# Optimization experiments

Hardware: AMD Instinct MI355X
Metric: run time of the kernel (lower is better)

Reference implementation:

```python
import jax, jax.numpy as jnp
import numpy as np

DIM = 1024
N_HEADS = 16
B, S = 2, 2048


def setup_inputs() -> dict:
    key = jax.random.key(0)
    ks = jax.random.split(key, 9)
    scale = 1.0 / np.sqrt(DIM)
    return {
        "i1": jax.random.normal(ks[0], (B, S, DIM), jnp.float32),
        "i2": jax.random.normal(ks[1], (B, S, DIM), jnp.float32),
        "cr": jax.random.normal(ks[2], (B, S, 2), jnp.float32),
        # Linear params stored as [in, out] so forward is x @ W + b (same math as torch x W^T + b)
        "Wq": jax.random.normal(ks[3], (DIM, DIM), jnp.float32) * scale,
        "bq": jnp.zeros((DIM,), jnp.float32),
        "Wkv": jax.random.normal(ks[4], (DIM, 2 * DIM), jnp.float32) * scale,
        "bkv": jnp.zeros((2 * DIM,), jnp.float32),
        "Wmo": jax.random.normal(ks[5], (2, DIM), jnp.float32) * (1.0 / np.sqrt(2.0)),
        "bmo": jnp.zeros((DIM,), jnp.float32),
    }


def reference(i1, i2, cr, Wq, bq, Wkv, bkv, Wmo, bmo):
    H = N_HEADS
    Dh = DIM // H
    b, s, _ = i1.shape

    q = (i1 @ Wq + bq).reshape(b, s, H, Dh)                # [B,S,H,Dh]
    kv = i2 @ Wkv + bkv                                     # [B,S,2*DIM]
    k = kv[..., :DIM].reshape(b, s, H, Dh)
    v = kv[..., DIM:].reshape(b, s, H, Dh)
    mo = (cr @ Wmo + bmo).reshape(b, s, H, Dh)              # [B,S,H,Dh]

    scores = jnp.einsum("bqhd,bkhd->bhqk", q, k) / jnp.sqrt(jnp.asarray(Dh, q.dtype))
    probs = jax.nn.softmax(scores, axis=-1)                 # [B,H,S,S] (dropout p=0)

    h = jnp.einsum("bhqk,bkhd->bqhd", probs, v).reshape(b, s, DIM)
    m = jnp.einsum("bhqk,bkhd->bqhd", probs, mo).reshape(b, s, DIM)
    return h, m
```

## Files before the change

kernel.cpp:

```cpp
#include <hip/hip_runtime.h>
#include <hip/hip_bf16.h>

typedef __attribute__((ext_vector_type(8))) short short8;
typedef __attribute__((ext_vector_type(4))) short short4_t;
typedef __attribute__((ext_vector_type(4))) float f32x4;
typedef unsigned short ushort_t;

#define DEV __device__ __forceinline__

DEV ushort_t f2bf(float f) {
    unsigned u = __builtin_bit_cast(unsigned, f);
    u = u + 0x7fffu + ((u >> 16) & 1u);
    return (ushort_t)(u >> 16);
}

DEV unsigned pk_bf16(float lo, float hi) {
    __hip_bfloat162 h = __float22bfloat162_rn(make_float2(lo, hi));
    unsigned u;
    __builtin_memcpy(&u, &h, sizeof(u));
    return u;
}

DEV float fast_exp2(float x) {
#if __has_builtin(__builtin_amdgcn_exp2f)
    return __builtin_amdgcn_exp2f(x);
#else
    float r;
    asm("v_exp_f32 %0, %1" : "=v"(r) : "v"(x));
    return r;
#endif
}

DEV short8 ld8(const ushort_t* p) { return *reinterpret_cast<const short8*>(p); }

#define SCL_F 0.18033688011112042f

__global__ __launch_bounds__(256)
void cvt_bf16(const float* __restrict__ in, ushort_t* __restrict__ out)
{
    const size_t i = ((size_t)blockIdx.x * 256 + threadIdx.x) * 8;
    const float4 a = *reinterpret_cast<const float4*>(in + i);
    const float4 b = *reinterpret_cast<const float4*>(in + i + 4);
    short8 v;
    v[0] = (short)f2bf(a.x); v[1] = (short)f2bf(a.y);
    v[2] = (short)f2bf(a.z); v[3] = (short)f2bf(a.w);
    v[4] = (short)f2bf(b.x); v[5] = (short)f2bf(b.y);
    v[6] = (short)f2bf(b.z); v[7] = (short)f2bf(b.w);
    *reinterpret_cast<short8*>(out + i) = v;
}

__global__ __launch_bounds__(256)
void tcvt_bf16(const float* __restrict__ W, ushort_t* __restrict__ Wt, int K, int N)
{
    __shared__ ushort_t tile[64][72];
    const int t = threadIdx.x;
    const int nx = blockIdx.x * 64, ky = blockIdx.y * 64;
    const int r = t >> 2, q = (t & 3) * 16;

    const float* src = W + (size_t)(ky + r) * N + nx + q;
#pragma unroll
    for (int i = 0; i < 4; ++i) {
        const float4 v = *reinterpret_cast<const float4*>(src + 4 * i);
        tile[r][q + 4 * i + 0] = f2bf(v.x);
        tile[r][q + 4 * i + 1] = f2bf(v.y);
        tile[r][q + 4 * i + 2] = f2bf(v.z);
        tile[r][q + 4 * i + 3] = f2bf(v.w);
    }
    __syncthreads();
    short8 o0, o1;
#pragma unroll
    for (int i = 0; i < 8; ++i) {
        o0[i] = (short)tile[q + i][r];
        o1[i] = (short)tile[q + 8 + i][r];
    }
    ushort_t* dst = Wt + (size_t)(nx + r) * K + ky + q;
    *reinterpret_cast<short8*>(dst) = o0;
    *reinterpret_cast<short8*>(dst + 8) = o1;
}

__global__ __launch_bounds__(256, 2)
void proj_all(const ushort_t* __restrict__ A1, const ushort_t* __restrict__ A2,
              const ushort_t* __restrict__ Wqt, const ushort_t* __restrict__ Wkvt,
              const float* __restrict__ bqv, const float* __restrict__ bkv,
              ushort_t* __restrict__ Qr, ushort_t* __restrict__ Kr,
              ushort_t* __restrict__ Vt)
{
    __shared__ ushort_t As[128 * 72];
    __shared__ ushort_t Bs[128 * 72];

    const int t = threadIdx.x;
    const int lane = t & 63;
    const int wv = t >> 6;
    const int wr = wv >> 1, wc = wv & 1;
    const int c = lane & 15, g = lane >> 4;
    const int m0 = blockIdx.y * 128;
    const int nblk = blockIdx.x;

    const ushort_t* A;
    const ushort_t* Wt;
    const float* bias;
    int n0;
    if (nblk < 8) { A = A1; Wt = Wqt;  bias = bqv; n0 = nblk * 128; }
    else          { A = A2; Wt = Wkvt; bias = bkv; n0 = (nblk - 8) * 128; }
    const bool isQ = (nblk < 8);
    const float qscale = isQ ? SCL_F : 1.0f;

    f32x4 acc[4][4];
    const f32x4 zero4 = {0.f, 0.f, 0.f, 0.f};
#pragma unroll
    for (int mi = 0; mi < 4; ++mi)
#pragma unroll
        for (int ni = 0; ni < 4; ++ni) acc[mi][ni] = zero4;

    const int srow[4] = { (t + 0)   >> 3, (t + 256) >> 3, (t + 512) >> 3, (t + 768) >> 3 };
    const int skq     = (t & 7) * 8;

    short8 a_reg[4], b_reg[4];
#pragma unroll
    for (int rep = 0; rep < 4; ++rep) {
        a_reg[rep] = ld8(A  + (size_t)(m0 + srow[rep]) * 1024 + skq);
        b_reg[rep] = ld8(Wt + (size_t)(n0 + srow[rep]) * 1024 + skq);
    }

    for (int it = 0; it < 16; ++it) {
#pragma unroll
        for (int rep = 0; rep < 4; ++rep) {
            *reinterpret_cast<short8*>(&As[srow[rep] * 72 + skq]) = a_reg[rep];
            *reinterpret_cast<short8*>(&Bs[srow[rep] * 72 + skq]) = b_reg[rep];
        }
        __syncthreads();
        if (it < 15) {
            const int k1 = (it + 1) * 64;
#pragma unroll
            for (int rep = 0; rep < 4; ++rep) {
                a_reg[rep] = ld8(A  + (size_t)(m0 + srow[rep]) * 1024 + k1 + skq);
                b_reg[rep] = ld8(Wt + (size_t)(n0 + srow[rep]) * 1024 + k1 + skq);
            }
        }
#pragma unroll
        for (int kk = 0; kk < 64; kk += 32) {
            short8 afr[4], bfr[4];
#pragma unroll
            for (int mi = 0; mi < 4; ++mi)
                afr[mi] = ld8(&As[(wr * 64 + mi * 16 + c) * 72 + kk + 8 * g]);
#pragma unroll
            for (int ni = 0; ni < 4; ++ni)
                bfr[ni] = ld8(&Bs[(wc * 64 + ni * 16 + c) * 72 + kk + 8 * g]);
#pragma unroll
            for (int mi = 0; mi < 4; ++mi)
#pragma unroll
                for (int ni = 0; ni < 4; ++ni)
                    acc[mi][ni] = __builtin_amdgcn_mfma_f32_16x16x32_bf16(
                        afr[mi], bfr[ni], acc[mi][ni], 0, 0, 0);
        }
        __syncthreads();
    }

#pragma unroll
    for (int mi = 0; mi < 4; ++mi) {
#pragma unroll
        for (int ni = 0; ni < 4; ++ni) {
            const int n = n0 + wc * 64 + ni * 16 + c;
            const float bb = bias[n];
#pragma unroll
            for (int j = 0; j < 4; ++j) {
                const int m = m0 + wr * 64 + mi * 16 + 4 * g + j;
                const int b = m >> 11, s = m & 2047;
                const ushort_t val = f2bf((acc[mi][ni][j] + bb) * qscale);
                if (isQ) {
                    Qr[((size_t)((b * 16 + (n >> 6)) * 2048 + s)) * 64 + (n & 63)] = val;
                } else if (n < 1024) {
                    Kr[((size_t)((b * 16 + (n >> 6)) * 2048 + s)) * 64 + (n & 63)] = val;
                } else {
                    const int np = n - 1024;
                    Vt[(size_t)((b * 16 + (np >> 6)) * 64 + (np & 63)) * 2048 + s] = val;
                }
            }
        }
    }
}

__global__ __launch_bounds__(256)
void proj_gemm(const float* __restrict__ A, const float* __restrict__ W,
               const float* __restrict__ bias, int N,
               ushort_t* __restrict__ outRow, ushort_t* __restrict__ outT)
{
    __shared__ ushort_t As[128 * 72];
    __shared__ ushort_t Bt[128 * 72];

    const int t = threadIdx.x;
    const int lane = t & 63;
    const int wv = t >> 6;
    const int wr = wv >> 1, wc = wv & 1;
    const int c = lane & 15, g = lane >> 4;
    const int m0 = blockIdx.y * 128, n0 = blockIdx.x * 128;
    const float qscale = (outT == nullptr) ? SCL_F : 1.0f;

    f32x4 acc[4][4];
    const f32x4 zero4 = {0.f, 0.f, 0.f, 0.f};
#pragma unroll
    for (int mi = 0; mi < 4; ++mi)
#pragma unroll
        for (int ni = 0; ni < 4; ++ni) acc[mi][ni] = zero4;

    for (int it = 0; it < 16; ++it) {
        const int k0 = it * 64;
        {
            const int kq = (t & 15) * 4;
            int r = t >> 4;
#pragma unroll
            for (int rep = 0; rep < 8; ++rep, r += 16) {
                float4 v = *reinterpret_cast<const float4*>(
                    A + (size_t)(m0 + r) * 1024 + k0 + kq);
                ushort_t* dst = &As[r * 72 + kq];
                dst[0] = f2bf(v.x); dst[1] = f2bf(v.y);
                dst[2] = f2bf(v.z); dst[3] = f2bf(v.w);
            }
        }
        {
            const int nq = (t & 31) * 4;
            const int kr = t >> 5;
#pragma unroll
            for (int rep = 0; rep < 8; ++rep) {
                const int k = kr + 8 * rep;
                float4 v = *reinterpret_cast<const float4*>(
                    W + (size_t)(k0 + k) * N + n0 + nq);
                Bt[(nq + 0) * 72 + k] = f2bf(v.x);
                Bt[(nq + 1) * 72 + k] = f2bf(v.y);
                Bt[(nq + 2) * 72 + k] = f2bf(v.z);
                Bt[(nq + 3) * 72 + k] = f2bf(v.w);
            }
        }
        __syncthreads();
#pragma unroll
        for (int kk = 0; kk < 64; kk += 32) {
            short8 afr[4], bfr[4];
#pragma unroll
            for (int mi = 0; mi < 4; ++mi)
                afr[mi] = ld8(&As[(wr * 64 + mi * 16 + c) * 72 + kk + 8 * g]);
#pragma unroll
            for (int ni = 0; ni < 4; ++ni)
                bfr[ni] = ld8(&Bt[(wc * 64 + ni * 16 + c) * 72 + kk + 8 * g]);
#pragma unroll
            for (int mi = 0; mi < 4; ++mi)
#pragma unroll
                for (int ni = 0; ni < 4; ++ni)
                    acc[mi][ni] = __builtin_amdgcn_mfma_f32_16x16x32_bf16(
                        afr[mi], bfr[ni], acc[mi][ni], 0, 0, 0);
        }
        __syncthreads();
    }

#pragma unroll
    for (int mi = 0; mi < 4; ++mi) {
#pragma unroll
        for (int ni = 0; ni < 4; ++ni) {
            const int n = n0 + wc * 64 + ni * 16 + c;
            const float bb = bias[n];
#pragma unroll
            for (int j = 0; j < 4; ++j) {
                const int m = m0 + wr * 64 + mi * 16 + 4 * g + j;
                const int b = m >> 11, s = m & 2047;
                const ushort_t val = f2bf((acc[mi][ni][j] + bb) * qscale);
                if (outT != nullptr && n >= 1024) {
                    const int np = n - 1024;
                    const int hh = np >> 6, d = np & 63;
                    outT[(size_t)((b * 16 + hh) * 64 + d) * 2048 + s] = val;
                } else {
                    const int hh = n >> 6, d = n & 63;
                    outRow[((size_t)((b * 16 + hh) * 2048 + s)) * 64 + d] = val;
                }
            }
        }
    }
}

DEV void tile_compute(const ushort_t* __restrict__ Ks, const ushort_t* __restrict__ Vs,
                      const ushort_t* __restrict__ Sts, int c, int g,
                      const short8 (&bq)[2][2],
                      f32x4 (&accv)[2][4], f32x4 (&stat)[2])
{
    const f32x4 zero4 = {0.f, 0.f, 0.f, 0.f};
    const int kxor = (c & 7) << 3;
    const int vxor = (c & 7) << 2;

    short8 KC[2][2];
#pragma unroll
    for (int ct = 0; ct < 2; ++ct)
#pragma unroll
        for (int st = 0; st < 2; ++st)
            KC[ct][st] = ld8(&Ks[(ct * 16 + c) * 64 + ((st * 32 + 8 * g) ^ kxor)]);
    short8 VC[4];
#pragma unroll
    for (int dt = 0; dt < 4; ++dt) {
        const short4_t vlo = *reinterpret_cast<const short4_t*>(
            &Vs[(dt * 16 + c) * 32 + ((4 * g) ^ vxor)]);
        const short4_t vhi = *reinterpret_cast<const short4_t*>(
            &Vs[(dt * 16 + c) * 32 + ((4 * g + 16) ^ vxor)]);
        VC[dt] = __builtin_shufflevector(vlo, vhi, 0, 1, 2, 3, 4, 5, 6, 7);
    }
    const short4_t slo = *reinterpret_cast<const short4_t*>(
        &Sts[c * 32 + ((4 * g) ^ vxor)]);
    const short4_t shi = *reinterpret_cast<const short4_t*>(
        &Sts[c * 32 + ((4 * g + 16) ^ vxor)]);
    const short8 stf = __builtin_shufflevector(slo, shi, 0, 1, 2, 3, 4, 5, 6, 7);

    f32x4 sc[2][2];
#pragma unroll
    for (int qt = 0; qt < 2; ++qt)
#pragma unroll
        for (int ct = 0; ct < 2; ++ct) {
            f32x4 z = zero4;
            z = __builtin_amdgcn_mfma_f32_16x16x32_bf16(KC[ct][0], bq[qt][0], z, 0, 0, 0);
            z = __builtin_amdgcn_mfma_f32_16x16x32_bf16(KC[ct][1], bq[qt][1], z, 0, 0, 0);
            sc[qt][ct] = z;
        }

    short8 pa[2];
#pragma unroll
    for (int qt = 0; qt < 2; ++qt) {
        float e[2][4];
#pragma unroll
        for (int ct = 0; ct < 2; ++ct)
#pragma unroll
            for (int j = 0; j < 4; ++j)
                e[ct][j] = fast_exp2(sc[qt][ct][j]);
        int4 w;
        w.x = (int)pk_bf16(e[0][0], e[0][1]);
        w.y = (int)pk_bf16(e[0][2], e[0][3]);
        w.z = (int)pk_bf16(e[1][0], e[1][1]);
        w.w = (int)pk_bf16(e[1][2], e[1][3]);
        pa[qt] = __builtin_bit_cast(short8, w);
    }

#pragma unroll
    for (int qt = 0; qt < 2; ++qt)
        stat[qt] = __builtin_amdgcn_mfma_f32_16x16x32_bf16(stf, pa[qt], stat[qt], 0, 0, 0);
#pragma unroll
    for (int dt = 0; dt < 4; ++dt) {
        accv[0][dt] = __builtin_amdgcn_mfma_f32_16x16x32_bf16(VC[dt], pa[0], accv[0][dt], 0, 0, 0);
        accv[1][dt] = __builtin_amdgcn_mfma_f32_16x16x32_bf16(VC[dt], pa[1], accv[1][dt], 0, 0, 0);
    }
}

DEV void pair_body(const ushort_t* __restrict__ Kh, const ushort_t* __restrict__ Vh,
                   const float* __restrict__ crb, int kvA, int kvB,
                   const ushort_t* KsC0, const ushort_t* VsC0, const ushort_t* StC0,
                   const ushort_t* KsC1, const ushort_t* VsC1, const ushort_t* StC1,
                   ushort_t* KsN0, ushort_t* VsN0, ushort_t* StN0,
                   ushort_t* KsN1, ushort_t* VsN1, ushort_t* StN1,
                   int t, int c, int g, int rk, int ck, int rv, int cv,
                   int kaddr, int vaddr0, int vaddr1,
                   const short8 (&bq)[2][2],
                   f32x4 (&accv)[2][4], f32x4 (&stat)[2])
{
    const short8 kregA = ld8(Kh + (size_t)(kvA + rk) * 64 + ck);
    const short8 vregA = ld8(Vh + (size_t)rv * 2048 + kvA + cv);
    const short8 kregB = ld8(Kh + (size_t)(kvB + rk) * 64 + ck);
    const short8 vregB = ld8(Vh + (size_t)rv * 2048 + kvB + cv);
    ushort_t crsh = 0; int staddr = 0;
    if (t < 128) {
        const int kvX = (t & 64) ? kvB : kvA;
        const int row = 1 + ((t >> 5) & 1);
        const float v = crb[(size_t)(kvX + (t & 31)) * 2 + (row - 1)];
        crsh = f2bf(v);
        staddr = row * 32 + ((t & 31) ^ ((row & 7) << 2));
    }
    __builtin_amdgcn_sched_barrier(0);

    tile_compute(KsC0, VsC0, StC0, c, g, bq, accv, stat);
    tile_compute(KsC1, VsC1, StC1, c, g, bq, accv, stat);

    *reinterpret_cast<short8*>(&KsN0[kaddr]) = kregA;
    *reinterpret_cast<short8*>(&KsN1[kaddr]) = kregB;
    *reinterpret_cast<short4_t*>(&VsN0[vaddr0]) = __builtin_shufflevector(vregA, vregA, 0, 1, 2, 3);
    *reinterpret_cast<short4_t*>(&VsN0[vaddr1]) = __builtin_shufflevector(vregA, vregA, 4, 5, 6, 7);
    *reinterpret_cast<short4_t*>(&VsN1[vaddr0]) = __builtin_shufflevector(vregB, vregB, 0, 1, 2, 3);
    *reinterpret_cast<short4_t*>(&VsN1[vaddr1]) = __builtin_shufflevector(vregB, vregB, 4, 5, 6, 7);
    if (t < 128) ((t & 64) ? StN1 : StN0)[staddr] = crsh;
    __syncthreads();
}

__global__ __launch_bounds__(256, 2)
void attn_kernel(const ushort_t* __restrict__ Qr, const ushort_t* __restrict__ Kr,
                 const ushort_t* __restrict__ Vt, const float* __restrict__ cr,
                 const float* __restrict__ Wmo, const float* __restrict__ bmo,
                 float* __restrict__ out)
{
    __shared__ ushort_t smem[18432];
    ushort_t* K0 = smem;            ushort_t* K1 = smem + 2048;
    ushort_t* K2 = smem + 4096;     ushort_t* K3 = smem + 6144;
    ushort_t* V0 = smem + 8192;     ushort_t* V1 = smem + 10240;
    ushort_t* V2 = smem + 12288;    ushort_t* V3 = smem + 14336;
    ushort_t* S0 = smem + 16384;    ushort_t* S1 = smem + 16896;
    ushort_t* S2 = smem + 17408;    ushort_t* S3 = smem + 17920;

    const int t = threadIdx.x;
    const int w = t >> 6, lane = t & 63;
    const int c = lane & 15, g = lane >> 4;
    const int rk = t >> 3, ck = (t & 7) * 8;
    const int rv = t >> 2, cv = (t & 3) * 8;
    const int kaddr  = rk * 64 + (ck ^ ((rk & 7) << 3));
    const int vaddr0 = rv * 32 + (cv ^ ((rv & 7) << 2));
    const int vaddr1 = rv * 32 + ((cv + 4) ^ ((rv & 7) << 2));

    const int gid = blockIdx.x;
    const int bh = (gid & 7) + 8 * ((gid >> 3) & 3);
    const int xt = gid >> 5;
    const int b = bh >> 4, hh = bh & 15;
    const int qb = xt * 128 + w * 32;

    const ushort_t* Qh = Qr + (size_t)bh * (2048 * 64);
    const ushort_t* Kh = Kr + (size_t)bh * (2048 * 64);
    const ushort_t* Vh = Vt + (size_t)bh * (64 * 2048);
    const float*   crb = cr + (size_t)b * (2048 * 2);

    short8 bq[2][2];
#pragma unroll
    for (int qt = 0; qt < 2; ++qt)
#pragma unroll
        for (int st = 0; st < 2; ++st)
            bq[qt][st] = ld8(Qh + (size_t)(qb + qt * 16 + c) * 64 + st * 32 + 8 * g);

    f32x4 accv[2][4];
    f32x4 stat[2];
    const f32x4 zero4 = {0.f, 0.f, 0.f, 0.f};
#pragma unroll
    for (int qt = 0; qt < 2; ++qt) {
        stat[qt] = zero4;
#pragma unroll
        for (int dt = 0; dt < 4; ++dt) accv[qt][dt] = zero4;
    }

    for (int idx = t; idx < 2048; idx += 256) {
        const int row = (idx >> 5) & 15;
        if (row != 1 && row != 2)
            smem[16384 + idx] = (row == 0) ? (ushort_t)0x3F80 : (ushort_t)0;
    }

    {
        const short8 kA = ld8(Kh + (size_t)rk * 64 + ck);
        const short8 vA = ld8(Vh + (size_t)rv * 2048 + cv);
        const short8 kB = ld8(Kh + (size_t)(32 + rk) * 64 + ck);
        const short8 vB = ld8(Vh + (size_t)rv * 2048 + 32 + cv);
        *reinterpret_cast<short8*>(&K0[kaddr]) = kA;
        *reinterpret_cast<short8*>(&K1[kaddr]) = kB;
        *reinterpret_cast<short4_t*>(&V0[vaddr0]) = __builtin_shufflevector(vA, vA, 0, 1, 2, 3);
        *reinterpret_cast<short4_t*>(&V0[vaddr1]) = __builtin_shufflevector(vA, vA, 4, 5, 6, 7);
        *reinterpret_cast<short4_t*>(&V1[vaddr0]) = __builtin_shufflevector(vB, vB, 0, 1, 2, 3);
        *reinterpret_cast<short4_t*>(&V1[vaddr1]) = __builtin_shufflevector(vB, vB, 4, 5, 6, 7);
        if (t < 128) {
            const int kvX = (t & 64) ? 32 : 0;
            const int row = 1 + ((t >> 5) & 1);
            const float v = crb[(size_t)(kvX + (t & 31)) * 2 + (row - 1)];
            ((t & 64) ? S1 : S0)[row * 32 + ((t & 31) ^ ((row & 7) << 2))] = f2bf(v);
        }
    }
    __syncthreads();

    for (int i = 0; i < 16; ++i) {
        const int base = i * 128;
        pair_body(Kh, Vh, crb, base + 64, base + 96,
                  K0, V0, S0, K1, V1, S1,
                  K2, V2, S2, K3, V3, S3,
                  t, c, g, rk, ck, rv, cv, kaddr, vaddr0, vaddr1,
                  bq, accv, stat);
        pair_body(Kh, Vh, crb, (base + 128) & 2047, (base + 160) & 2047,
                  K2, V2, S2, K3, V3, S3,
                  K0, V0, S0, K1, V1, S1,
                  t, c, g, rk, ck, rv, cv, kaddr, vaddr0, vaddr1,
                  bq, accv, stat);
    }

    float lst[2], a0s[2], a1s[2];
#pragma unroll
    for (int qt = 0; qt < 2; ++qt) {
        lst[qt] = __shfl(stat[qt][0], c, 64);
        a0s[qt] = __shfl(stat[qt][1], c, 64);
        a1s[qt] = __shfl(stat[qt][2], c, 64);
    }

#pragma unroll
    for (int qt = 0; qt < 2; ++qt) {
        const int q = qb + qt * 16 + c;
        const float inv = 1.f / lst[qt];
        const float a0 = a0s[qt] * inv, a1 = a1s[qt] * inv;
#pragma unroll
        for (int dt = 0; dt < 4; ++dt) {
            const int d = hh * 64 + dt * 16 + 4 * g;
            const float4 w0 = *reinterpret_cast<const float4*>(Wmo + d);
            const float4 w1 = *reinterpret_cast<const float4*>(Wmo + 1024 + d);
            const float4 bm = *reinterpret_cast<const float4*>(bmo + d);
            const size_t oidx = ((size_t)(b * 2048 + q)) * 1024 + d;
            float4 hv, mv;
            hv.x = accv[qt][dt][0] * inv; hv.y = accv[qt][dt][1] * inv;
            hv.z = accv[qt][dt][2] * inv; hv.w = accv[qt][dt][3] * inv;
            mv.x = a0 * w0.x + a1 * w1.x + bm.x;
            mv.y = a0 * w0.y + a1 * w1.y + bm.y;
            mv.z = a0 * w0.z + a1 * w1.z + bm.z;
            mv.w = a0 * w0.w + a1 * w1.w + bm.w;
            *reinterpret_cast<float4*>(out + oidx) = hv;
            *reinterpret_cast<float4*>(out + 4194304 + oidx) = mv;
        }
    }
}

extern "C" void kernel_launch(void* const* d_in, const int* in_sizes, int n_in,
                              void* d_out, int out_size, void* d_ws, size_t ws_size,
                              hipStream_t stream)
{
    const float* i1  = (const float*)d_in[0];
    const float* i2  = (const float*)d_in[1];
    const float* cr  = (const float*)d_in[2];
    const float* Wq  = (const float*)d_in[3];
    const float* bq  = (const float*)d_in[4];
    const float* Wkv = (const float*)d_in[5];
    const float* bkv = (const float*)d_in[6];
    const float* Wmo = (const float*)d_in[7];
    const float* bmo = (const float*)d_in[8];
    float* out = (float*)d_out;

    ushort_t* Qr = (ushort_t*)d_ws;
    ushort_t* Kr = Qr + 4194304;
    ushort_t* Vt = Kr + 4194304;

    if (ws_size >= 48234496ULL) {
        ushort_t* A1   = Vt + 4194304;
        ushort_t* A2   = A1 + 4194304;
        ushort_t* Wqt  = A2 + 4194304;
        ushort_t* Wkvt = Wqt + 1048576;
        cvt_bf16<<<dim3(2048), dim3(256), 0, stream>>>(i1, A1);
        cvt_bf16<<<dim3(2048), dim3(256), 0, stream>>>(i2, A2);
        tcvt_bf16<<<dim3(16, 16), dim3(256), 0, stream>>>(Wq, Wqt, 1024, 1024);
        tcvt_bf16<<<dim3(32, 16), dim3(256), 0, stream>>>(Wkv, Wkvt, 1024, 2048);
        proj_all<<<dim3(24, 32), dim3(256), 0, stream>>>(A1, A2, Wqt, Wkvt, bq, bkv, Qr, Kr, Vt);
    } else {
        proj_gemm<<<dim3(8, 32), dim3(256), 0, stream>>>(i1, Wq, bq, 1024, Qr, nullptr);
        proj_gemm<<<dim3(16, 32), dim3(256), 0, stream>>>(i2, Wkv, bkv, 2048, Kr, Vt);
    }
    attn_kernel<<<dim3(512), dim3(256), 0, stream>>>(Qr, Kr, Vt, cr, Wmo, bmo, out);
}
```

Before: 115.7 us.

## Fuse fp32-to-bf16 activation conversion into projection GEMM and add MFMA priority hints

Drops the two standalone cvt_bf16 kernels. proj_all now loads fp32 activations directly and packs them to bf16 while staging them into shared memory, which removes a full write and re-read of two 16 MB-scale intermediates plus two launches. The cost is that proj_all reloads fp32 A tiles from global memory for each of its 24 column blocks, doubling the A-tile bytes per load and raising register pressure for the prefetch. The attention inner loop also wraps its MFMA sections in s_setprio to favour matrix issue over the exp and pack work.

Result: slower. 119.1 us (+2.9%).

```diff
diff --git a/kernel.cpp b/kernel.cpp
--- a/kernel.cpp
+++ b/kernel.cpp
@@ -36,20 +36,6 @@
 #define SCL_F 0.18033688011112042f
 
 __global__ __launch_bounds__(256)
-void cvt_bf16(const float* __restrict__ in, ushort_t* __restrict__ out)
-{
-    const size_t i = ((size_t)blockIdx.x * 256 + threadIdx.x) * 8;
-    const float4 a = *reinterpret_cast<const float4*>(in + i);
-    const float4 b = *reinterpret_cast<const float4*>(in + i + 4);
-    short8 v;
-    v[0] = (short)f2bf(a.x); v[1] = (short)f2bf(a.y);
-    v[2] = (short)f2bf(a.z); v[3] = (short)f2bf(a.w);
-    v[4] = (short)f2bf(b.x); v[5] = (short)f2bf(b.y);
-    v[6] = (short)f2bf(b.z); v[7] = (short)f2bf(b.w);
-    *reinterpret_cast<short8*>(out + i) = v;
-}
-
-__global__ __launch_bounds__(256)
 void tcvt_bf16(const float* __restrict__ W, ushort_t* __restrict__ Wt, int K, int N)
 {
     __shared__ ushort_t tile[64][72];
@@ -79,7 +65,7 @@
 }
 
 __global__ __launch_bounds__(256, 2)
-void proj_all(const ushort_t* __restrict__ A1, const ushort_t* __restrict__ A2,
+void proj_all(const float* __restrict__ i1, const float* __restrict__ i2,
               const ushort_t* __restrict__ Wqt, const ushort_t* __restrict__ Wkvt,
               const float* __restrict__ bqv, const float* __restrict__ bkv,
               ushort_t* __restrict__ Qr, ushort_t* __restrict__ Kr,
@@ -96,12 +82,12 @@
     const int m0 = blockIdx.y * 128;
     const int nblk = blockIdx.x;
 
-    const ushort_t* A;
+    const float* Af;
     const ushort_t* Wt;
     const float* bias;
     int n0;
-    if (nblk < 8) { A = A1; Wt = Wqt;  bias = bqv; n0 = nblk * 128; }
-    else          { A = A2; Wt = Wkvt; bias = bkv; n0 = (nblk - 8) * 128; }
+    if (nblk < 8) { Af = i1; Wt = Wqt;  bias = bqv; n0 = nblk * 128; }
+    else          { Af = i2; Wt = Wkvt; bias = bkv; n0 = (nblk - 8) * 128; }
     const bool isQ = (nblk < 8);
     const float qscale = isQ ? SCL_F : 1.0f;
 
@@ -115,17 +101,26 @@
     const int srow[4] = { (t + 0)   >> 3, (t + 256) >> 3, (t + 512) >> 3, (t + 768) >> 3 };
     const int skq     = (t & 7) * 8;
 
-    short8 a_reg[4], b_reg[4];
+    float4 a_lo[4], a_hi[4];
+    short8 b_reg[4];
 #pragma unroll
     for (int rep = 0; rep < 4; ++rep) {
-        a_reg[rep] = ld8(A  + (size_t)(m0 + srow[rep]) * 1024 + skq);
+        const float* src = Af + (size_t)(m0 + srow[rep]) * 1024 + skq;
+        a_lo[rep] = *reinterpret_cast<const float4*>(src);
+        a_hi[rep] = *reinterpret_cast<const float4*>(src + 4);
         b_reg[rep] = ld8(Wt + (size_t)(n0 + srow[rep]) * 1024 + skq);
     }
 
     for (int it = 0; it < 16; ++it) {
 #pragma unroll
         for (int rep = 0; rep < 4; ++rep) {
-            *reinterpret_cast<short8*>(&As[srow[rep] * 72 + skq]) = a_reg[rep];
+            int4 wvp;
+            wvp.x = (int)pk_bf16(a_lo[rep].x, a_lo[rep].y);
+            wvp.y = (int)pk_bf16(a_lo[rep].z, a_lo[rep].w);
+            wvp.z = (int)pk_bf16(a_hi[rep].x, a_hi[rep].y);
+            wvp.w = (int)pk_bf16(a_hi[rep].z, a_hi[rep].w);
+            *reinterpret_cast<short8*>(&As[srow[rep] * 72 + skq]) =
+                __builtin_bit_cast(short8, wvp);
             *reinterpret_cast<short8*>(&Bs[srow[rep] * 72 + skq]) = b_reg[rep];
         }
         __syncthreads();
@@ -133,7 +128,9 @@
             const int k1 = (it + 1) * 64;
 #pragma unroll
             for (int rep = 0; rep < 4; ++rep) {
-                a_reg[rep] = ld8(A  + (size_t)(m0 + srow[rep]) * 1024 + k1 + skq);
+                const float* src = Af + (size_t)(m0 + srow[rep]) * 1024 + k1 + skq;
+                a_lo[rep] = *reinterpret_cast<const float4*>(src);
+                a_hi[rep] = *reinterpret_cast<const float4*>(src + 4);
                 b_reg[rep] = ld8(Wt + (size_t)(n0 + srow[rep]) * 1024 + k1 + skq);
             }
         }
@@ -306,6 +303,7 @@
     const short8 stf = __builtin_shufflevector(slo, shi, 0, 1, 2, 3, 4, 5, 6, 7);
 
     f32x4 sc[2][2];
+    __builtin_amdgcn_s_setprio(1);
 #pragma unroll
     for (int qt = 0; qt < 2; ++qt)
 #pragma unroll
@@ -315,6 +313,7 @@
             z = __builtin_amdgcn_mfma_f32_16x16x32_bf16(KC[ct][1], bq[qt][1], z, 0, 0, 0);
             sc[qt][ct] = z;
         }
+    __builtin_amdgcn_s_setprio(0);
 
     short8 pa[2];
 #pragma unroll
@@ -333,6 +332,7 @@
         pa[qt] = __builtin_bit_cast(short8, w);
     }
 
+    __builtin_amdgcn_s_setprio(1);
 #pragma unroll
     for (int qt = 0; qt < 2; ++qt)
         stat[qt] = __builtin_amdgcn_mfma_f32_16x16x32_bf16(stf, pa[qt], stat[qt], 0, 0, 0);
@@ -341,6 +341,7 @@
         accv[0][dt] = __builtin_amdgcn_mfma_f32_16x16x32_bf16(VC[dt], pa[0], accv[0][dt], 0, 0, 0);
         accv[1][dt] = __builtin_amdgcn_mfma_f32_16x16x32_bf16(VC[dt], pa[1], accv[1][dt], 0, 0, 0);
     }
+    __builtin_amdgcn_s_setprio(0);
 }
 
 DEV void pair_body(const ushort_t* __restrict__ Kh, const ushort_t* __restrict__ Vh,
@@ -524,16 +525,12 @@
     ushort_t* Kr = Qr + 4194304;
     ushort_t* Vt = Kr + 4194304;
 
-    if (ws_size >= 48234496ULL) {
-        ushort_t* A1   = Vt + 4194304;
-        ushort_t* A2   = A1 + 4194304;
-        ushort_t* Wqt  = A2 + 4194304;
+    if (ws_size >= 31457280ULL) {
+        ushort_t* Wqt  = Vt + 4194304;
         ushort_t* Wkvt = Wqt + 1048576;
-        cvt_bf16<<<dim3(2048), dim3(256), 0, stream>>>(i1, A1);
-        cvt_bf16<<<dim3(2048), dim3(256), 0, stream>>>(i2, A2);
         tcvt_bf16<<<dim3(16, 16), dim3(256), 0, stream>>>(Wq, Wqt, 1024, 1024);
         tcvt_bf16<<<dim3(32, 16), dim3(256), 0, stream>>>(Wkv, Wkvt, 1024, 2048);
-        proj_all<<<dim3(24, 32), dim3(256), 0, stream>>>(A1, A2, Wqt, Wkvt, bq, bkv, Qr, Kr, Vt);
+        proj_all<<<dim3(24, 32), dim3(256), 0, stream>>>(i1, i2, Wqt, Wkvt, bq, bkv, Qr, Kr, Vt);
     } else {
         proj_gemm<<<dim3(8, 32), dim3(256), 0, stream>>>(i1, Wq, bq, 1024, Qr, nullptr);
         proj_gemm<<<dim3(16, 32), dim3(256), 0, stream>>>(i2, Wkv, bkv, 2048, Kr, Vt);
```
